# Kernel optimization log

Measured on AMD Instinct MI355X. Metric: run time of the kernel, lower is better.

## Reference

```python
import jax, jax.numpy as jnp
import numpy as np

N, E, F_IN, H, L = 50000, 200000, 16, 128, 3
EPS = 1e-5

def _glorot(key, shape):
    fan_in, fan_out = shape[0], shape[1]
    lim = (6.0 / (fan_in + fan_out)) ** 0.5
    return jax.random.uniform(key, shape, jnp.float32, -lim, lim)

def setup_inputs() -> dict:
    key = jax.random.key(0)
    ks = jax.random.split(key, 16)
    d = {}
    d['x'] = jax.random.normal(ks[0], (N, F_IN), jnp.float32)
    d['edge_index'] = jax.random.randint(ks[1], (2, E), 0, N, jnp.int32)
    d['edge_attr'] = jax.random.normal(ks[2], (E, F_IN), jnp.float32)
    # encoder (Linear+ReLU to hidden)
    d['enc_node_w'] = _glorot(ks[3], (F_IN, H)); d['enc_node_b'] = jnp.zeros((H,), jnp.float32)
    d['enc_edge_w'] = _glorot(ks[4], (F_IN, H)); d['enc_edge_b'] = jnp.zeros((H,), jnp.float32)
    # 3 meta layers, stacked along leading axis
    d['edge_w'] = jnp.stack([_glorot(jax.random.fold_in(ks[5], i), (3 * H, H)) for i in range(L)])
    d['edge_b'] = jnp.zeros((L, H), jnp.float32)
    d['n1_w'] = jnp.stack([_glorot(jax.random.fold_in(ks[6], i), (2 * H, H)) for i in range(L)])
    d['n1_b'] = jnp.zeros((L, H), jnp.float32)
    d['n2_w'] = jnp.stack([_glorot(jax.random.fold_in(ks[7], i), (2 * H, H)) for i in range(L)])
    d['n2_b'] = jnp.zeros((L, H), jnp.float32)
    # shared batch norms (training-mode batch statistics)
    d['bn_node_g'] = jnp.ones((H,), jnp.float32); d['bn_node_b'] = jnp.zeros((H,), jnp.float32)
    d['bn_edge_g'] = jnp.ones((H,), jnp.float32); d['bn_edge_b'] = jnp.zeros((H,), jnp.float32)
    d['reg_w'] = _glorot(ks[8], (2 * H, 1)); d['reg_b'] = jnp.zeros((1,), jnp.float32)
    return d

def _segment_mean(data, idx, n):
    s = jax.ops.segment_sum(data, idx, num_segments=n)
    cnt = jax.ops.segment_sum(jnp.ones((idx.shape[0], 1), data.dtype), idx, num_segments=n)
    return s / jnp.maximum(cnt, 1.0)

def _bn(v, g, b):
    m = v.mean(0)
    var = v.var(0)  # biased, matches torch BN training normalization
    return (v - m) * jax.lax.rsqrt(var + EPS) * g + b

def reference(x, edge_index, edge_attr, enc_node_w, enc_node_b, enc_edge_w, enc_edge_b,
              edge_w, edge_b, n1_w, n1_b, n2_w, n2_b,
              bn_node_g, bn_node_b, bn_edge_g, bn_edge_b, reg_w, reg_b):
    row, col = edge_index[0], edge_index[1]
    h = jax.nn.relu(x @ enc_node_w + enc_node_b)          # [N,H]
    e = jax.nn.relu(edge_attr @ enc_edge_w + enc_edge_b)  # [E,H]
    n_nodes = h.shape[0]
    for i in range(L):
        # EdgeModel: phi_e(concat(src, dst, e))
        e = jax.nn.relu(jnp.concatenate([h[row], h[col], e], 1) @ edge_w[i] + edge_b[i])
        # NodeModel: mlp1(concat(x[row], e)) -> scatter-mean over col -> mlp2(concat(x, agg))
        m = jax.nn.relu(jnp.concatenate([h[row], e], 1) @ n1_w[i] + n1_b[i])
        agg = _segment_mean(m, col, n_nodes)
        h = jax.nn.relu(jnp.concatenate([h, agg], 1) @ n2_w[i] + n2_b[i])
        if i < L - 1:
            h = _bn(h, bn_node_g, bn_node_b)
            e = _bn(e, bn_edge_g, bn_edge_b)
    readout = jnp.concatenate([h.mean(0, keepdims=True), e.mean(0, keepdims=True)], 1)  # [1,2H]
    return readout @ reg_w + reg_b  # [1,1]
```

## Files before the change

kernel.cpp:

```cpp
#include <hip/hip_runtime.h>

#define H 128
#define F_IN 16
#define BNEPS 1e-5f

typedef __attribute__((ext_vector_type(8))) short short8;
typedef __attribute__((ext_vector_type(4))) float f32x4;

__device__ __forceinline__ unsigned short f2bf(float f)
{
    unsigned u = __builtin_bit_cast(unsigned, f);
    u += 0x7FFFu + ((u >> 16) & 1u);
    return (unsigned short)(u >> 16);
}
__device__ __forceinline__ float bf2f(unsigned short h)
{
    return __builtin_bit_cast(float, (unsigned)h << 16);
}

__device__ __forceinline__ void bn_param(const float* __restrict__ S,
                                         const float* __restrict__ g,
                                         const float* __restrict__ b,
                                         float invM, int j,
                                         float* __restrict__ sS, float* __restrict__ sT)
{
    float s = 1.f, tt = 0.f;
    if (S) {
        float mean = S[j] * invM;
        float var  = S[H + j] * invM - mean * mean;
        s  = rsqrtf(var + BNEPS) * g[j];
        tt = b[j] - mean * s;
    }
    sS[j] = s;
    sT[j] = tt;
}

__device__ __forceinline__ void stage_aff(const unsigned short* __restrict__ src,
                                          unsigned short* sA, int r0, int M, int t,
                                          const float* __restrict__ sS,
                                          const float* __restrict__ sT)
{
#pragma unroll
    for (int i = 0; i < 4; ++i) {
        int cid  = t + 256 * i;
        int row  = cid >> 4;
        int ck   = cid & 15;
        int grow = r0 + row;
        short8 v = (short8)0;
        if (grow < M) {
            v = *(const short8*)(src + (size_t)grow * H + ck * 8);
            int j0 = ck * 8;
#pragma unroll
            for (int j = 0; j < 8; ++j)
                v[j] = (short)f2bf(bf2f((unsigned short)v[j]) * sS[j0 + j] + sT[j0 + j]);
        }
        *(short8*)(sA + (row << 7) + ((ck ^ (row & 7)) << 3)) = v;
    }
}

__device__ __forceinline__ void stage_aff_gather(const unsigned short* __restrict__ src,
                                                 const int* __restrict__ idx,
                                                 unsigned short* sA, int p0, int M, int t,
                                                 const float* __restrict__ sS,
                                                 const float* __restrict__ sT)
{
#pragma unroll
    for (int i = 0; i < 4; ++i) {
        int cid = t + 256 * i;
        int row = cid >> 4;
        int ck  = cid & 15;
        int p   = p0 + row;
        short8 v = (short8)0;
        if (p < M) {
            v = *(const short8*)(src + (size_t)idx[p] * H + ck * 8);
            int j0 = ck * 8;
#pragma unroll
            for (int j = 0; j < 8; ++j)
                v[j] = (short)f2bf(bf2f((unsigned short)v[j]) * sS[j0 + j] + sT[j0 + j]);
        }
        *(short8*)(sA + (row << 7) + ((ck ^ (row & 7)) << 3)) = v;
    }
}

__device__ __forceinline__ void stage_agg_bf16(float* __restrict__ aggsum,
                                               unsigned short* sA, int r0, int M, int t)
{
#pragma unroll
    for (int i = 0; i < 4; ++i) {
        int cid  = t + 256 * i;
        int row  = cid >> 4;
        int ck   = cid & 15;
        int grow = r0 + row;
        short8 ph = (short8)0;
        if (grow < M) {
            float4* q = (float4*)(aggsum + (size_t)grow * H + ck * 8);
            float4 a = q[0], b = q[1];
            float xs[8] = {a.x, a.y, a.z, a.w, b.x, b.y, b.z, b.w};
#pragma unroll
            for (int j = 0; j < 8; ++j) ph[j] = (short)f2bf(xs[j]);
            q[0] = make_float4(0.f, 0.f, 0.f, 0.f);
            q[1] = make_float4(0.f, 0.f, 0.f, 0.f);
        }
        *(short8*)(sA + (row << 7) + ((ck ^ (row & 7)) << 3)) = ph;
    }
}

__global__ __launch_bounds__(256) void wbf16_kernel(const float* __restrict__ edge_w,
                                                    const float* __restrict__ n1_w,
                                                    const float* __restrict__ n2_w,
                                                    short8* __restrict__ out)
{
    int m = blockIdx.x;
    int layer = m / 7, k = m % 7;
    const float* W = (k < 3) ? edge_w + (size_t)layer * 384 * H + (size_t)k * H * H
                   : (k < 5) ? n1_w + (size_t)layer * 256 * H + (size_t)(k - 3) * H * H
                             : n2_w + (size_t)layer * 256 * H + (size_t)(k - 5) * H * H;
    short8* oh = out + (size_t)m * 2048;
    for (int e = threadIdx.x; e < 2048; e += 256) {
        int jbB = e >> 9, s = (e >> 7) & 3, c = (e >> 6) & 1, lane = e & 63;
        int g = lane >> 4, c0 = lane & 15;
        short8 hi;
#pragma unroll
        for (int j = 0; j < 8; ++j)
            hi[j] = (short)f2bf(W[(size_t)(32 * s + 8 * g + j) * H + jbB * 32 + 16 * c + c0]);
        oh[e] = hi;
    }
}

__device__ __forceinline__ void load_wfrag(const short8* __restrict__ Wp, int jbB,
                                           int lane, short8 wf[4][2])
{
#pragma unroll
    for (int s = 0; s < 4; ++s)
#pragma unroll
        for (int c = 0; c < 2; ++c)
            wf[s][c] = Wp[((jbB * 4 + s) * 2 + c) * 64 + lane];
}

__device__ __forceinline__ void mfma_gemm(const unsigned short* sA, const short8 wf[4][2],
                                          f32x4 acc[4][2], int lane)
{
    const int g = lane >> 4, r = lane & 15;
#pragma unroll
    for (int s = 0; s < 4; ++s) {
        short8 a4[4];
#pragma unroll
        for (int fr = 0; fr < 4; ++fr) {
            int row = 16 * fr + r;
            int ck  = (4 * s + g) ^ (row & 7);
            a4[fr] = *(const short8*)(sA + (row << 7) + (ck << 3));
        }
#pragma unroll
        for (int fr = 0; fr < 4; ++fr)
#pragma unroll
            for (int c = 0; c < 2; ++c)
                acc[fr][c] = __builtin_amdgcn_mfma_f32_16x16x32_bf16(a4[fr], wf[s][c],
                                                                     acc[fr][c], 0, 0, 0);
    }
}

__device__ __forceinline__ void zero_acc(f32x4 acc[4][2])
{
#pragma unroll
    for (int fr = 0; fr < 4; ++fr)
#pragma unroll
        for (int c = 0; c < 2; ++c) {
            acc[fr][c][0] = 0.f; acc[fr][c][1] = 0.f;
            acc[fr][c][2] = 0.f; acc[fr][c][3] = 0.f;
        }
}

__global__ __launch_bounds__(256) void hist_kernel(const int* __restrict__ col,
                                                   int* __restrict__ cnt, int E)
{
    int e = blockIdx.x * 256 + threadIdx.x;
    if (e < E) atomicAdd(&cnt[col[e]], 1);
}

__global__ __launch_bounds__(1024) void scan_kernel(const int* __restrict__ cnt,
                                                    int* __restrict__ offs, int Nn)
{
    __shared__ int ls[1024];
    int t = threadIdx.x;
    int per = (Nn + 1023) / 1024;
    int base = t * per;
    int s = 0;
    for (int k = 0; k < per; ++k) {
        int i = base + k;
        if (i < Nn) s += cnt[i];
    }
    ls[t] = s;
    __syncthreads();
    for (int d = 1; d < 1024; d <<= 1) {
        int u = (t >= d) ? ls[t - d] : 0;
        __syncthreads();
        ls[t] += u;
        __syncthreads();
    }
    int run = ls[t] - s;
    for (int k = 0; k < per; ++k) {
        int i = base + k;
        if (i < Nn) {
            offs[i] = run;
            run += cnt[i];
        }
    }
}

__global__ __launch_bounds__(256) void scatter_kernel(const int* __restrict__ row,
                                                      const int* __restrict__ col,
                                                      const int* __restrict__ offs,
                                                      int* __restrict__ tmpc,
                                                      int* __restrict__ sortedIds,
                                                      int* __restrict__ rowS,
                                                      int* __restrict__ colS, int E)
{
    int e = blockIdx.x * 256 + threadIdx.x;
    if (e < E) {
        int c = col[e];
        int p = offs[c] + atomicAdd(&tmpc[c], 1);
        sortedIds[p] = e;
        rowS[p] = row[e];
        colS[p] = c;
    }
}

__global__ __launch_bounds__(256) void enc_kernel(const float* __restrict__ X,
                                                  const float* __restrict__ W,
                                                  const float* __restrict__ bias,
                                                  unsigned short* __restrict__ out, int M)
{
    __shared__ float sW[F_IN * H];
    __shared__ float sb[H];
    int t = threadIdx.x;
    reinterpret_cast<float4*>(sW)[t]       = reinterpret_cast<const float4*>(W)[t];
    reinterpret_cast<float4*>(sW)[t + 256] = reinterpret_cast<const float4*>(W)[t + 256];
    if (t < H) sb[t] = bias[t];
    __syncthreads();
    int row = blockIdx.x * 2 + (t >> 7);
    if (row >= M) return;
    int j = t & 127;
    float acc = sb[j];
#pragma unroll
    for (int k = 0; k < F_IN; ++k)
        acc += X[(size_t)row * F_IN + k] * sW[k * H + j];
    out[(size_t)row * H + j] = f2bf(fmaxf(acc, 0.f));
}

__global__ __launch_bounds__(256) void enc_gather_kernel(const float* __restrict__ X,
                                                         const int* __restrict__ sortedIds,
                                                         const float* __restrict__ W,
                                                         const float* __restrict__ bias,
                                                         unsigned short* __restrict__ out,
                                                         int M)
{
    __shared__ float sW[F_IN * H];
    __shared__ float sb[H];
    int t = threadIdx.x;
    reinterpret_cast<float4*>(sW)[t]       = reinterpret_cast<const float4*>(W)[t];
    reinterpret_cast<float4*>(sW)[t + 256] = reinterpret_cast<const float4*>(W)[t + 256];
    if (t < H) sb[t] = bias[t];
    __syncthreads();
    int p = blockIdx.x * 2 + (t >> 7);
    if (p >= M) return;
    int src = sortedIds[p];
    int j = t & 127;
    float acc = sb[j];
#pragma unroll
    for (int k = 0; k < F_IN; ++k)
        acc += X[(size_t)src * F_IN + k] * sW[k * H + j];
    out[(size_t)p * H + j] = f2bf(fmaxf(acc, 0.f));
}

__global__ __launch_bounds__(256, 3) void edge_kernel(unsigned short* eb,
                                                      const int* __restrict__ rowS,
                                                      const int* __restrict__ colS,
                                                      const int* __restrict__ cnt,
                                                      const unsigned short* __restrict__ hb,
                                                      const short8* __restrict__ wfrL,
                                                      const float* __restrict__ be,
                                                      const float* __restrict__ b1,
                                                      float* __restrict__ aggsum, int E,
                                                      const float* __restrict__ Sh,
                                                      const float* __restrict__ gh,
                                                      const float* __restrict__ bh,
                                                      float invN,
                                                      const float* __restrict__ Se,
                                                      const float* __restrict__ ge,
                                                      const float* __restrict__ beB,
                                                      float invE,
                                                      float* __restrict__ eStats)
{
    __shared__ __align__(16) unsigned char smem[64 * 128 * 6 + 256 + 256 + 2048];
    unsigned short* sE  = (unsigned short*)smem;
    unsigned short* sHt = sE + 64 * 128;
    unsigned short* sHc = sHt + 64 * 128;
    float*          mbuf = (float*)smem;
    int*            scol = (int*)(smem + 64 * 128 * 6);
    float*          sinv = (float*)(smem + 64 * 128 * 6 + 256);
    float*          bnp  = (float*)(smem + 64 * 128 * 6 + 512);

    const int t = threadIdx.x, lane = t & 63, w = t >> 6, jb = 32 * w;
    const int e0 = blockIdx.x * 64;
    const int g = lane >> 4, c0 = lane & 15;

    if (t < 64) {
        int cc = colS[(e0 + t < E) ? (e0 + t) : (E - 1)];
        scol[t] = cc;
        int c = cnt[cc];
        sinv[t] = 1.f / (float)(c > 1 ? c : 1);
    }
    if (t < 128) bn_param(Sh, gh, bh, invN, t, bnp, bnp + 128);
    else         bn_param(Se, ge, beB, invE, t - 128, bnp + 256, bnp + 384);
    __syncthreads();

    stage_aff(eb, sE, e0, E, t, bnp + 256, bnp + 384);
    stage_aff_gather(hb, rowS, sHt, e0, E, t, bnp, bnp + 128);
    stage_aff_gather(hb, scol - 0, sHc, 0, E - e0 > 64 ? 64 : (E - e0), t, bnp, bnp + 128);

    short8 wf[4][2];
    f32x4 acc[4][2];
    zero_acc(acc);
    load_wfrag(wfrL + 2 * 2048, w, lane, wf);
    __syncthreads();
    mfma_gemm(sE, wf, acc, lane);
    load_wfrag(wfrL + 0 * 2048, w, lane, wf);
    mfma_gemm(sHt, wf, acc, lane);
    load_wfrag(wfrL + 1 * 2048, w, lane, wf);
    mfma_gemm(sHc, wf, acc, lane);
    __syncthreads();

    float s1[2] = {0.f, 0.f}, s2[2] = {0.f, 0.f};
#pragma unroll
    for (int fr = 0; fr < 4; ++fr)
#pragma unroll
        for (int c = 0; c < 2; ++c) {
            int j = jb + 16 * c + c0;
            float bej = be[j];
#pragma unroll
            for (int r = 0; r < 4; ++r) {
                int Rl = 16 * fr + 4 * g + r;
                int p  = e0 + Rl;
                float v = acc[fr][c][r] + bej;
                v = fmaxf(v, 0.f);
                unsigned short vb = f2bf(v);
                if (p < E) {
                    eb[(size_t)p * H + j] = vb;
                    s1[c] += v;
                    s2[c] += v * v;
                }
                sE[(Rl << 7) + (j ^ ((Rl & 7) << 3))] = vb;
            }
        }
    __syncthreads();

    zero_acc(acc);
    load_wfrag(wfrL + 4 * 2048, w, lane, wf);
    mfma_gemm(sE, wf, acc, lane);
    load_wfrag(wfrL + 3 * 2048, w, lane, wf);
    mfma_gemm(sHt, wf, acc, lane);
    __syncthreads();

#pragma unroll
    for (int fr = 0; fr < 4; ++fr)
#pragma unroll
        for (int c = 0; c < 2; ++c) {
            int j = jb + 16 * c + c0;
            float b1j = b1[j];
#pragma unroll
            for (int r = 0; r < 4; ++r) {
                int Rl = 16 * fr + 4 * g + r;
                float v = fmaxf(acc[fr][c][r] + b1j, 0.f);
                mbuf[(Rl << 7) + (j ^ (((Rl >> 2) & 3) << 3))] = v;
            }
        }
    __syncthreads();

    {
        int j = t & 127, half = t >> 7;
        int rbeg = half * 32, rend = rbeg + 32;
        int rlim = E - e0;
        float run = 0.f;
        int cur = scol[rbeg];
        for (int row = rbeg; row < rend; ++row) {
            int cc = scol[row];
            float v = mbuf[(row << 7) + (j ^ (((row >> 2) & 3) << 3))];
            if (cc != cur) {
                if (run != 0.f)
                    atomicAdd(&aggsum[(size_t)cur * H + j], run * sinv[row - 1]);
                run = 0.f;
                cur = cc;
            }
            if (row < rlim) run += v;
        }
        if (run != 0.f)
            atomicAdd(&aggsum[(size_t)cur * H + j], run * sinv[rend - 1]);
    }

#pragma unroll
    for (int c = 0; c < 2; ++c) {
        float a = s1[c], b = s2[c];
        a += __shfl_xor(a, 16); a += __shfl_xor(a, 32);
        b += __shfl_xor(b, 16); b += __shfl_xor(b, 32);
        if (g == 0) {
            int j = jb + 16 * c + c0;
            atomicAdd(&eStats[j], a);
            atomicAdd(&eStats[H + j], b);
        }
    }
}

__global__ __launch_bounds__(256, 5) void node_kernel(unsigned short* hb,
                                                      float* __restrict__ aggsum,
                                                      const short8* __restrict__ wfrL,
                                                      const float* __restrict__ b2, int M,
                                                      const float* __restrict__ Sh,
                                                      const float* __restrict__ gh,
                                                      const float* __restrict__ bh,
                                                      float invN,
                                                      float* __restrict__ hStats)
{
    __shared__ __align__(16) unsigned short sA[64 * 128];
    __shared__ __align__(16) unsigned short sB[64 * 128];
    __shared__ float bnp[256];
    const int t = threadIdx.x, lane = t & 63, w = t >> 6, jb = 32 * w;
    const int r0 = blockIdx.x * 64;
    if (t < 128) bn_param(Sh, gh, bh, invN, t, bnp, bnp + 128);
    __syncthreads();
    stage_aff(hb, sA, r0, M, t, bnp, bnp + 128);
    stage_agg_bf16(aggsum, sB, r0, M, t);
    short8 wf[4][2];
    f32x4 acc[4][2];
    zero_acc(acc);
    load_wfrag(wfrL + 5 * 2048, w, lane, wf);
    __syncthreads();
    mfma_gemm(sA, wf, acc, lane);
    load_wfrag(wfrL + 6 * 2048, w, lane, wf);
    mfma_gemm(sB, wf, acc, lane);
    const int g = lane >> 4, c0 = lane & 15;
    float s1[2] = {0.f, 0.f}, s2[2] = {0.f, 0.f};
#pragma unroll
    for (int fr = 0; fr < 4; ++fr)
#pragma unroll
        for (int c = 0; c < 2; ++c) {
            int j = jb + 16 * c + c0;
            float bj = b2[j];
#pragma unroll
            for (int r = 0; r < 4; ++r) {
                int row = r0 + 16 * fr + 4 * g + r;
                if (row < M) {
                    float v = fmaxf(acc[fr][c][r] + bj, 0.f);
                    hb[(size_t)row * H + j] = f2bf(v);
                    s1[c] += v;
                    s2[c] += v * v;
                }
            }
        }
#pragma unroll
    for (int c = 0; c < 2; ++c) {
        float a = s1[c], b = s2[c];
        a += __shfl_xor(a, 16); a += __shfl_xor(a, 32);
        b += __shfl_xor(b, 16); b += __shfl_xor(b, 32);
        if (g == 0) {
            int j = jb + 16 * c + c0;
            atomicAdd(&hStats[j], a);
            atomicAdd(&hStats[H + j], b);
        }
    }
}

__global__ __launch_bounds__(256) void final_kernel(const float* __restrict__ hsum,
                                                    const float* __restrict__ esum,
                                                    const float* __restrict__ reg_w,
                                                    const float* __restrict__ reg_b,
                                                    float* __restrict__ out,
                                                    float invN, float invE)
{
    __shared__ float red[256];
    int t = threadIdx.x;
    float v = (t < 128) ? hsum[t] * invN * reg_w[t]
                        : esum[t - 128] * invE * reg_w[t];
    red[t] = v;
    __syncthreads();
    for (int s = 128; s > 0; s >>= 1) {
        if (t < s) red[t] += red[t + s];
        __syncthreads();
    }
    if (t == 0) out[0] = red[0] + reg_b[0];
}

extern "C" void kernel_launch(void* const* d_in, const int* in_sizes, int n_in,
                              void* d_out, int out_size, void* d_ws, size_t ws_size,
                              hipStream_t stream)
{
    const float* x          = (const float*)d_in[0];
    const int*   edge_index = (const int*)  d_in[1];
    const float* edge_attr  = (const float*)d_in[2];
    const float* enc_node_w = (const float*)d_in[3];
    const float* enc_node_b = (const float*)d_in[4];
    const float* enc_edge_w = (const float*)d_in[5];
    const float* enc_edge_b = (const float*)d_in[6];
    const float* edge_w     = (const float*)d_in[7];
    const float* edge_b     = (const float*)d_in[8];
    const float* n1_w       = (const float*)d_in[9];
    const float* n1_b       = (const float*)d_in[10];
    const float* n2_w       = (const float*)d_in[11];
    const float* n2_b       = (const float*)d_in[12];
    const float* bn_node_g  = (const float*)d_in[13];
    const float* bn_node_b  = (const float*)d_in[14];
    const float* bn_edge_g  = (const float*)d_in[15];
    const float* bn_edge_b  = (const float*)d_in[16];
    const float* reg_w      = (const float*)d_in[17];
    const float* reg_b      = (const float*)d_in[18];

    const int N = in_sizes[0] / F_IN;
    const int E = in_sizes[1] / 2;
    const size_t NH = (size_t)N * H;
    const size_t EH = (size_t)E * H;

    float* ws     = (float*)d_ws;
    float* aggsum = ws;
    float* statsA = aggsum + NH;
    float* statsB = statsA + 512;
    short8* wfr   = (short8*)(statsB + 512);
    unsigned short* hbuf = (unsigned short*)(wfr + 21 * 2048);
    unsigned short* ebuf = hbuf + NH;
    int*   cnt_i  = (int*)(ebuf + EH);
    int*   tmpc   = cnt_i + N;
    int*   offs   = tmpc + N;
    int*   sortedIds = offs + N + 1;
    int*   rowS   = sortedIds + E;
    int*   colS   = rowS + E;

    const int* row_idx = edge_index;
    const int* col_idx = edge_index + E;
    const float invN = 1.f / (float)N;
    const float invE = 1.f / (float)E;

    (void)hipMemsetAsync(cnt_i, 0, (size_t)2 * N * sizeof(int), stream);
    (void)hipMemsetAsync(aggsum, 0, NH * sizeof(float), stream);
    hist_kernel<<<(E + 255) / 256, 256, 0, stream>>>(col_idx, cnt_i, E);
    scan_kernel<<<1, 1024, 0, stream>>>(cnt_i, offs, N);
    scatter_kernel<<<(E + 255) / 256, 256, 0, stream>>>(row_idx, col_idx, offs, tmpc,
                                                        sortedIds, rowS, colS, E);
    wbf16_kernel<<<21, 256, 0, stream>>>(edge_w, n1_w, n2_w, wfr);

    enc_kernel<<<(N + 1) / 2, 256, 0, stream>>>(x, enc_node_w, enc_node_b, hbuf, N);
    enc_gather_kernel<<<(E + 1) / 2, 256, 0, stream>>>(edge_attr, sortedIds,
                                                       enc_edge_w, enc_edge_b, ebuf, E);

    const int nodeBlocks = (N + 63) / 64;
    const int edgeBlocks = (E + 63) / 64;

    for (int i = 0; i < 3; ++i) {
        float*       Scur  = (i & 1) ? statsB : statsA;
        const float* Sprev = (i == 0) ? nullptr : ((i & 1) ? statsA : statsB);
        const float* Sh = Sprev;
        const float* Se = Sprev ? Sprev + 256 : nullptr;
        const short8* wfrL = wfr + (size_t)i * 7 * 2048;
        (void)hipMemsetAsync(Scur, 0, 512 * sizeof(float), stream);
        edge_kernel<<<edgeBlocks, 256, 0, stream>>>(
            ebuf, rowS, colS, cnt_i, hbuf, wfrL,
            edge_b + i * H, n1_b + i * H,
            aggsum, E,
            Sh, bn_node_g, bn_node_b, invN,
            Se, bn_edge_g, bn_edge_b, invE,
            Scur + 256);
        node_kernel<<<nodeBlocks, 256, 0, stream>>>(
            hbuf, aggsum, wfrL, n2_b + i * H, N,
            Sh, bn_node_g, bn_node_b, invN,
            Scur);
    }
    final_kernel<<<1, 256, 0, stream>>>(statsA, statsA + 256, reg_w, reg_b,
                                        (float*)d_out, invN, invE);
}
```

Before: 798.2 us.

## Use 512-thread blocks with each wave computing 16 output columns

Edge and node kernels now launch 8 waves per 64-row tile instead of 4. Each wave owns one 16-column output slice and holds half the accumulators and weight fragments, and staging and segmented-reduction loops are split across the larger block. The aim is more waves in flight to hide gather and LDS latency and lower register pressure per thread. In exchange, each A-fragment LDS read now feeds half as many MFMAs, and more threads contend at each barrier.

Measured after the change: 746.9 us. 6.4% less time.

```diff
diff --git a/kernel.cpp b/kernel.cpp
--- a/kernel.cpp
+++ b/kernel.cpp
@@ -41,8 +41,8 @@
                                           const float* __restrict__ sT)
 {
 #pragma unroll
-    for (int i = 0; i < 4; ++i) {
-        int cid  = t + 256 * i;
+    for (int i = 0; i < 2; ++i) {
+        int cid  = t + 512 * i;
         int row  = cid >> 4;
         int ck   = cid & 15;
         int grow = r0 + row;
@@ -65,8 +65,8 @@
                                                  const float* __restrict__ sT)
 {
 #pragma unroll
-    for (int i = 0; i < 4; ++i) {
-        int cid = t + 256 * i;
+    for (int i = 0; i < 2; ++i) {
+        int cid = t + 512 * i;
         int row = cid >> 4;
         int ck  = cid & 15;
         int p   = p0 + row;
@@ -86,8 +86,8 @@
                                                unsigned short* sA, int r0, int M, int t)
 {
 #pragma unroll
-    for (int i = 0; i < 4; ++i) {
-        int cid  = t + 256 * i;
+    for (int i = 0; i < 2; ++i) {
+        int cid  = t + 512 * i;
         int row  = cid >> 4;
         int ck   = cid & 15;
         int grow = r0 + row;
@@ -127,18 +127,17 @@
     }
 }
 
-__device__ __forceinline__ void load_wfrag(const short8* __restrict__ Wp, int jbB,
-                                           int lane, short8 wf[4][2])
-{
+__device__ __forceinline__ void load_wfrag_h(const short8* __restrict__ Wp, int w,
+                                             int lane, short8 wf[4])
+{
+    int base = ((w >> 1) * 8 + (w & 1)) * 64 + lane;
 #pragma unroll
     for (int s = 0; s < 4; ++s)
-#pragma unroll
-        for (int c = 0; c < 2; ++c)
-            wf[s][c] = Wp[((jbB * 4 + s) * 2 + c) * 64 + lane];
-}
-
-__device__ __forceinline__ void mfma_gemm(const unsigned short* sA, const short8 wf[4][2],
-                                          f32x4 acc[4][2], int lane)
+        wf[s] = Wp[base + s * 128];
+}
+
+__device__ __forceinline__ void mfma_gemm_h(const unsigned short* sA, const short8 wf[4],
+                                            f32x4 acc[4], int lane)
 {
     const int g = lane >> 4, r = lane & 15;
 #pragma unroll
@@ -152,22 +151,16 @@
         }
 #pragma unroll
         for (int fr = 0; fr < 4; ++fr)
-#pragma unroll
-            for (int c = 0; c < 2; ++c)
-                acc[fr][c] = __builtin_amdgcn_mfma_f32_16x16x32_bf16(a4[fr], wf[s][c],
-                                                                     acc[fr][c], 0, 0, 0);
-    }
-}
-
-__device__ __forceinline__ void zero_acc(f32x4 acc[4][2])
-{
-#pragma unroll
-    for (int fr = 0; fr < 4; ++fr)
-#pragma unroll
-        for (int c = 0; c < 2; ++c) {
-            acc[fr][c][0] = 0.f; acc[fr][c][1] = 0.f;
-            acc[fr][c][2] = 0.f; acc[fr][c][3] = 0.f;
-        }
+            acc[fr] = __builtin_amdgcn_mfma_f32_16x16x32_bf16(a4[fr], wf[s], acc[fr], 0, 0, 0);
+    }
+}
+
+__device__ __forceinline__ void zero_acc_h(f32x4 acc[4])
+{
+#pragma unroll
+    for (int fr = 0; fr < 4; ++fr) {
+        acc[fr][0] = 0.f; acc[fr][1] = 0.f; acc[fr][2] = 0.f; acc[fr][3] = 0.f;
+    }
 }
 
 __global__ __launch_bounds__(256) void hist_kernel(const int* __restrict__ col,
@@ -272,7 +265,7 @@
     out[(size_t)p * H + j] = f2bf(fmaxf(acc, 0.f));
 }
 
-__global__ __launch_bounds__(256, 3) void edge_kernel(unsigned short* eb,
+__global__ __launch_bounds__(512, 3) void edge_kernel(unsigned short* eb,
                                                       const int* __restrict__ rowS,
                                                       const int* __restrict__ colS,
                                                       const int* __restrict__ cnt,
@@ -300,9 +293,10 @@
     float*          sinv = (float*)(smem + 64 * 128 * 6 + 256);
     float*          bnp  = (float*)(smem + 64 * 128 * 6 + 512);
 
-    const int t = threadIdx.x, lane = t & 63, w = t >> 6, jb = 32 * w;
+    const int t = threadIdx.x, lane = t & 63, w = t >> 6;
     const int e0 = blockIdx.x * 64;
     const int g = lane >> 4, c0 = lane & 15;
+    const int j = 16 * w + c0;
 
     if (t < 64) {
         int cc = colS[(e0 + t < E) ? (e0 + t) : (E - 1)];
@@ -310,107 +304,104 @@
         int c = cnt[cc];
         sinv[t] = 1.f / (float)(c > 1 ? c : 1);
     }
-    if (t < 128) bn_param(Sh, gh, bh, invN, t, bnp, bnp + 128);
-    else         bn_param(Se, ge, beB, invE, t - 128, bnp + 256, bnp + 384);
+    if (t >= 64 && t < 192)      bn_param(Sh, gh, bh, invN, t - 64, bnp, bnp + 128);
+    else if (t >= 192 && t < 320) bn_param(Se, ge, beB, invE, t - 192, bnp + 256, bnp + 384);
     __syncthreads();
 
     stage_aff(eb, sE, e0, E, t, bnp + 256, bnp + 384);
     stage_aff_gather(hb, rowS, sHt, e0, E, t, bnp, bnp + 128);
-    stage_aff_gather(hb, scol - 0, sHc, 0, E - e0 > 64 ? 64 : (E - e0), t, bnp, bnp + 128);
-
-    short8 wf[4][2];
-    f32x4 acc[4][2];
-    zero_acc(acc);
-    load_wfrag(wfrL + 2 * 2048, w, lane, wf);
-    __syncthreads();
-    mfma_gemm(sE, wf, acc, lane);
-    load_wfrag(wfrL + 0 * 2048, w, lane, wf);
-    mfma_gemm(sHt, wf, acc, lane);
-    load_wfrag(wfrL + 1 * 2048, w, lane, wf);
-    mfma_gemm(sHc, wf, acc, lane);
-    __syncthreads();
-
-    float s1[2] = {0.f, 0.f}, s2[2] = {0.f, 0.f};
-#pragma unroll
-    for (int fr = 0; fr < 4; ++fr)
-#pragma unroll
-        for (int c = 0; c < 2; ++c) {
-            int j = jb + 16 * c + c0;
-            float bej = be[j];
+    {
+        int Mt = E - e0; if (Mt > 64) Mt = 64;
+        stage_aff_gather(hb, scol, sHc, 0, Mt, t, bnp, bnp + 128);
+    }
+
+    short8 wf[4];
+    f32x4 acc[4];
+    zero_acc_h(acc);
+    load_wfrag_h(wfrL + 2 * 2048, w, lane, wf);
+    __syncthreads();
+    mfma_gemm_h(sE, wf, acc, lane);
+    load_wfrag_h(wfrL + 0 * 2048, w, lane, wf);
+    mfma_gemm_h(sHt, wf, acc, lane);
+    load_wfrag_h(wfrL + 1 * 2048, w, lane, wf);
+    mfma_gemm_h(sHc, wf, acc, lane);
+    __syncthreads();
+
+    float s1 = 0.f, s2 = 0.f;
+    {
+        float bej = be[j];
+#pragma unroll
+        for (int fr = 0; fr < 4; ++fr)
 #pragma unroll
             for (int r = 0; r < 4; ++r) {
                 int Rl = 16 * fr + 4 * g + r;
                 int p  = e0 + Rl;
-                float v = acc[fr][c][r] + bej;
+                float v = acc[fr][r] + bej;
                 v = fmaxf(v, 0.f);
                 unsigned short vb = f2bf(v);
                 if (p < E) {
                     eb[(size_t)p * H + j] = vb;
-                    s1[c] += v;
-                    s2[c] += v * v;
+                    s1 += v;
+                    s2 += v * v;
                 }
                 sE[(Rl << 7) + (j ^ ((Rl & 7) << 3))] = vb;
             }
-        }
-    __syncthreads();
-
-    zero_acc(acc);
-    load_wfrag(wfrL + 4 * 2048, w, lane, wf);
-    mfma_gemm(sE, wf, acc, lane);
-    load_wfrag(wfrL + 3 * 2048, w, lane, wf);
-    mfma_gemm(sHt, wf, acc, lane);
-    __syncthreads();
-
-#pragma unroll
-    for (int fr = 0; fr < 4; ++fr)
-#pragma unroll
-        for (int c = 0; c < 2; ++c) {
-            int j = jb + 16 * c + c0;
-            float b1j = b1[j];
+    }
+    __syncthreads();
+
+    zero_acc_h(acc);
+    load_wfrag_h(wfrL + 4 * 2048, w, lane, wf);
+    mfma_gemm_h(sE, wf, acc, lane);
+    load_wfrag_h(wfrL + 3 * 2048, w, lane, wf);
+    mfma_gemm_h(sHt, wf, acc, lane);
+    __syncthreads();
+
+    {
+        float b1j = b1[j];
+#pragma unroll
+        for (int fr = 0; fr < 4; ++fr)
 #pragma unroll
             for (int r = 0; r < 4; ++r) {
                 int Rl = 16 * fr + 4 * g + r;
-                float v = fmaxf(acc[fr][c][r] + b1j, 0.f);
+                float v = fmaxf(acc[fr][r] + b1j, 0.f);
                 mbuf[(Rl << 7) + (j ^ (((Rl >> 2) & 3) << 3))] = v;
             }
-        }
-    __syncthreads();
-
-    {
-        int j = t & 127, half = t >> 7;
-        int rbeg = half * 32, rend = rbeg + 32;
+    }
+    __syncthreads();
+
+    {
+        int jc = t & 127, q = t >> 7;
+        int rbeg = q * 16, rend = rbeg + 16;
         int rlim = E - e0;
         float run = 0.f;
         int cur = scol[rbeg];
         for (int row = rbeg; row < rend; ++row) {
             int cc = scol[row];
-            float v = mbuf[(row << 7) + (j ^ (((row >> 2) & 3) << 3))];
+            float v = mbuf[(row << 7) + (jc ^ (((row >> 2) & 3) << 3))];
             if (cc != cur) {
                 if (run != 0.f)
-                    atomicAdd(&aggsum[(size_t)cur * H + j], run * sinv[row - 1]);
+                    atomicAdd(&aggsum[(size_t)cur * H + jc], run * sinv[row - 1]);
                 run = 0.f;
                 cur = cc;
             }
             if (row < rlim) run += v;
         }
         if (run != 0.f)
-            atomicAdd(&aggsum[(size_t)cur * H + j], run * sinv[rend - 1]);
-    }
-
-#pragma unroll
-    for (int c = 0; c < 2; ++c) {
-        float a = s1[c], b = s2[c];
+            atomicAdd(&aggsum[(size_t)cur * H + jc], run * sinv[rend - 1]);
+    }
+
+    {
+        float a = s1, b = s2;
         a += __shfl_xor(a, 16); a += __shfl_xor(a, 32);
         b += __shfl_xor(b, 16); b += __shfl_xor(b, 32);
         if (g == 0) {
-            int j = jb + 16 * c + c0;
             atomicAdd(&eStats[j], a);
             atomicAdd(&eStats[H + j], b);
         }
     }
 }
 
-__global__ __launch_bounds__(256, 5) void node_kernel(unsigned short* hb,
+__global__ __launch_bounds__(512, 4) void node_kernel(unsigned short* hb,
                                                       float* __restrict__ aggsum,
                                                       const short8* __restrict__ wfrL,
                                                       const float* __restrict__ b2, int M,
@@ -423,46 +414,43 @@
     __shared__ __align__(16) unsigned short sA[64 * 128];
     __shared__ __align__(16) unsigned short sB[64 * 128];
     __shared__ float bnp[256];
-    const int t = threadIdx.x, lane = t & 63, w = t >> 6, jb = 32 * w;
+    const int t = threadIdx.x, lane = t & 63, w = t >> 6;
     const int r0 = blockIdx.x * 64;
+    const int g = lane >> 4, c0 = lane & 15;
+    const int j = 16 * w + c0;
     if (t < 128) bn_param(Sh, gh, bh, invN, t, bnp, bnp + 128);
     __syncthreads();
     stage_aff(hb, sA, r0, M, t, bnp, bnp + 128);
     stage_agg_bf16(aggsum, sB, r0, M, t);
-    short8 wf[4][2];
-    f32x4 acc[4][2];
-    zero_acc(acc);
-    load_wfrag(wfrL + 5 * 2048, w, lane, wf);
-    __syncthreads();
-    mfma_gemm(sA, wf, acc, lane);
-    load_wfrag(wfrL + 6 * 2048, w, lane, wf);
-    mfma_gemm(sB, wf, acc, lane);
-    const int g = lane >> 4, c0 = lane & 15;
-    float s1[2] = {0.f, 0.f}, s2[2] = {0.f, 0.f};
-#pragma unroll
-    for (int fr = 0; fr < 4; ++fr)
-#pragma unroll
-        for (int c = 0; c < 2; ++c) {
-            int j = jb + 16 * c + c0;
-            float bj = b2[j];
+    short8 wf[4];
+    f32x4 acc[4];
+    zero_acc_h(acc);
+    load_wfrag_h(wfrL + 5 * 2048, w, lane, wf);
+    __syncthreads();
+    mfma_gemm_h(sA, wf, acc, lane);
+    load_wfrag_h(wfrL + 6 * 2048, w, lane, wf);
+    mfma_gemm_h(sB, wf, acc, lane);
+    float s1 = 0.f, s2 = 0.f;
+    {
+        float bj = b2[j];
+#pragma unroll
+        for (int fr = 0; fr < 4; ++fr)
 #pragma unroll
             for (int r = 0; r < 4; ++r) {
                 int row = r0 + 16 * fr + 4 * g + r;
                 if (row < M) {
-                    float v = fmaxf(acc[fr][c][r] + bj, 0.f);
+                    float v = fmaxf(acc[fr][r] + bj, 0.f);
                     hb[(size_t)row * H + j] = f2bf(v);
-                    s1[c] += v;
-                    s2[c] += v * v;
+                    s1 += v;
+                    s2 += v * v;
                 }
             }
-        }
-#pragma unroll
-    for (int c = 0; c < 2; ++c) {
-        float a = s1[c], b = s2[c];
+    }
+    {
+        float a = s1, b = s2;
         a += __shfl_xor(a, 16); a += __shfl_xor(a, 32);
         b += __shfl_xor(b, 16); b += __shfl_xor(b, 32);
         if (g == 0) {
-            int j = jb + 16 * c + c0;
             atomicAdd(&hStats[j], a);
             atomicAdd(&hStats[H + j], b);
         }
@@ -559,14 +547,14 @@
         const float* Se = Sprev ? Sprev + 256 : nullptr;
         const short8* wfrL = wfr + (size_t)i * 7 * 2048;
         (void)hipMemsetAsync(Scur, 0, 512 * sizeof(float), stream);
-        edge_kernel<<<edgeBlocks, 256, 0, stream>>>(
+        edge_kernel<<<edgeBlocks, 512, 0, stream>>>(
             ebuf, rowS, colS, cnt_i, hbuf, wfrL,
             edge_b + i * H, n1_b + i * H,
             aggsum, E,
             Sh, bn_node_g, bn_node_b, invN,
             Se, bn_edge_g, bn_edge_b, invE,
             Scur + 256);
-        node_kernel<<<nodeBlocks, 256, 0, stream>>>(
+        node_kernel<<<nodeBlocks, 512, 0, stream>>>(
             hbuf, aggsum, wfrL, n2_b + i * H, N,
             Sh, bn_node_g, bn_node_b, invN,
             Scur);
```
